# Optimization experiments

Measured on AMD Instinct MI355X. Metric: run time of the kernel, lower is better.

The kernel has to match this reference:

```python
import jax, jax.numpy as jnp
import numpy as np

HEAD_DIM = 512 // (8 * 2)  # in_dim // (num_heads * 2) = 32
SQRT2 = np.sqrt(2.0).astype(np.float32)


def dwt1d_haar(x):
    # Haar DWT along last dim: L=(even+odd)/sqrt2, H=(even-odd)/sqrt2
    xe, xo = x[..., 0::2], x[..., 1::2]
    return (xe + xo) / SQRT2, (xe - xo) / SQRT2


def idwt1d_haar(L, H):
    # Inverse: even=(L+H)/sqrt2, odd=(L-H)/sqrt2, interleaved
    even = (L + H) / SQRT2
    odd = (L - H) / SQRT2
    x = jnp.stack([even, odd], axis=-1)  # [..., D/2, 2]
    return x.reshape(*x.shape[:-2], -1)  # [..., D]


def setup_inputs() -> dict:
    key = jax.random.key(0)
    k1, k2, k3, k4 = jax.random.split(key, 4)
    B, S, D = 8, 2048, 512
    queries = jax.random.normal(k1, (B, S, D), dtype=jnp.float32)
    keys = jax.random.normal(k2, (B, S, D), dtype=jnp.float32)
    values = jax.random.normal(k3, (B, S, D), dtype=jnp.float32)
    W_o = jax.random.normal(k4, (D, D), dtype=jnp.float32) * (1.0 / np.sqrt(D))
    b_o = jnp.zeros((D,), dtype=jnp.float32)
    return {"queries": queries, "keys": keys, "values": values, "W_o": W_o, "b_o": b_o}


def reference(queries, keys, values, W_o, b_o):
    scale = 1.0 / jnp.sqrt(jnp.asarray(HEAD_DIM, dtype=queries.dtype))
    q_L, q_H = dwt1d_haar(queries)
    k_L, k_H = dwt1d_haar(keys)
    v_L, v_H = dwt1d_haar(values)
    # [B,S,S] score matrices for each wavelet branch
    attn_L = jax.nn.softmax(jnp.einsum("bqd,bkd->bqk", q_L, k_L) * scale, axis=-1)
    attn_H = jax.nn.softmax(jnp.einsum("bqd,bkd->bqk", q_H, k_H) * scale, axis=-1)
    L_out = jnp.einsum("bqk,bkd->bqd", attn_L, v_L)
    H_out = jnp.einsum("bqk,bkd->bqd", attn_H, v_H)
    output = idwt1d_haar(L_out, H_out)  # [B,S,D]
    return output @ W_o.T + b_o
```

## Files before the change

### kernel.cpp

```cpp
#include <hip/hip_runtime.h>

#define INV_SQRT2 0.70710678118654752f
#define QSCALE    0.17677669529663689f
#define LOG2E     1.44269504088896340f
#define SM_HALF   16.0f

typedef __attribute__((ext_vector_type(8))) short bf16x8;
typedef __attribute__((ext_vector_type(4))) float f32x4;
typedef __attribute__((ext_vector_type(16))) float f32x16;

__device__ __forceinline__ unsigned cvt_pk_bf16(float a, float b) {
  unsigned r;
  asm("v_cvt_pk_bf16_f32 %0, %1, %2" : "=v"(r) : "v"(a), "v"(b));
  return r;
}

__device__ __forceinline__ float exp2_raw(float x) {
  float r;
  asm("v_exp_f32 %0, %1" : "=v"(r) : "v"(x));
  return r;
}

__device__ __forceinline__ void async16(const short* g, short* l) {
  typedef __attribute__((address_space(3))) unsigned lds_u32;
  typedef const __attribute__((address_space(1))) unsigned glb_u32;
  __builtin_amdgcn_global_load_lds((glb_u32*)g, (lds_u32*)l, 16, 0, 0);
}

__launch_bounds__(256, 4)
__global__ void dwt_all(const float* __restrict__ q, const float* __restrict__ k,
                        const float* __restrict__ v, const float* __restrict__ W,
                        short* __restrict__ qs, short* __restrict__ ks,
                        short* __restrict__ vt, short* __restrict__ w2) {
  __shared__ float tL[32][65];
  __shared__ float tH[32][65];
  int bi = blockIdx.x;
  int t = threadIdx.x;
  if (bi < 2048) {
    int idx = bi * 256 + t;
    int j = idx & 31;
    int s = (idx >> 5) & 2047;
    int b = idx >> 16;
    const float4* qp = (const float4*)(q + ((size_t)(b * 2048 + s)) * 512 + j * 16);
    const float4* kp = (const float4*)(k + ((size_t)(b * 2048 + s)) * 512 + j * 16);
    float4 a0 = qp[0], a1 = qp[1], a2 = qp[2], a3 = qp[3];
    float4 c0 = kp[0], c1 = kp[1], c2 = kp[2], c3 = kp[3];
    union { bf16x8 v; unsigned u[4]; } qL, qH, kL, kH;
    const float cs = INV_SQRT2 * QSCALE * LOG2E;
    qL.u[0] = cvt_pk_bf16((a0.x + a0.y) * cs, (a0.z + a0.w) * cs);
    qL.u[1] = cvt_pk_bf16((a1.x + a1.y) * cs, (a1.z + a1.w) * cs);
    qL.u[2] = cvt_pk_bf16((a2.x + a2.y) * cs, (a2.z + a2.w) * cs);
    qL.u[3] = cvt_pk_bf16((a3.x + a3.y) * cs, (a3.z + a3.w) * cs);
    qH.u[0] = cvt_pk_bf16((a0.x - a0.y) * cs, (a0.z - a0.w) * cs);
    qH.u[1] = cvt_pk_bf16((a1.x - a1.y) * cs, (a1.z - a1.w) * cs);
    qH.u[2] = cvt_pk_bf16((a2.x - a2.y) * cs, (a2.z - a2.w) * cs);
    qH.u[3] = cvt_pk_bf16((a3.x - a3.y) * cs, (a3.z - a3.w) * cs);
    kL.u[0] = cvt_pk_bf16((c0.x + c0.y) * INV_SQRT2, (c0.z + c0.w) * INV_SQRT2);
    kL.u[1] = cvt_pk_bf16((c1.x + c1.y) * INV_SQRT2, (c1.z + c1.w) * INV_SQRT2);
    kL.u[2] = cvt_pk_bf16((c2.x + c2.y) * INV_SQRT2, (c2.z + c2.w) * INV_SQRT2);
    kL.u[3] = cvt_pk_bf16((c3.x + c3.y) * INV_SQRT2, (c3.z + c3.w) * INV_SQRT2);
    kH.u[0] = cvt_pk_bf16((c0.x - c0.y) * INV_SQRT2, (c0.z - c0.w) * INV_SQRT2);
    kH.u[1] = cvt_pk_bf16((c1.x - c1.y) * INV_SQRT2, (c1.z - c1.w) * INV_SQRT2);
    kH.u[2] = cvt_pk_bf16((c2.x - c2.y) * INV_SQRT2, (c2.z - c2.w) * INV_SQRT2);
    kH.u[3] = cvt_pk_bf16((c3.x - c3.y) * INV_SQRT2, (c3.z - c3.w) * INV_SQRT2);
    size_t oL = ((size_t)(b * 2) * 2048 + s) * 256 + j * 8;
    size_t oH = oL + (size_t)2048 * 256;
    *(bf16x8*)(qs + oL) = qL.v;  *(bf16x8*)(qs + oH) = qH.v;
    *(bf16x8*)(ks + oL) = kL.v;  *(bf16x8*)(ks + oH) = kH.v;
  } else if (bi < 4096) {
    int bi2 = bi - 2048;
    int it = bi2 & 3, st = (bi2 >> 2) & 63, b = bi2 >> 8;
#pragma unroll
    for (int rep = 0; rep < 4; rep++) {
      int unit = rep * 256 + t;
      int r = unit >> 5, cp = (unit & 31) * 2;
      float4 vv = *(const float4*)(v + ((size_t)(b * 2048 + st * 32 + r)) * 512 + it * 128 + cp * 2);
      tL[r][cp]     = (vv.x + vv.y) * INV_SQRT2;
      tL[r][cp + 1] = (vv.z + vv.w) * INV_SQRT2;
      tH[r][cp]     = (vv.x - vv.y) * INV_SQRT2;
      tH[r][cp + 1] = (vv.z - vv.w) * INV_SQRT2;
    }
    __syncthreads();
    {
      int i = t >> 2, cc = t & 3;
      union { bf16x8 v; unsigned u[4]; } pL, pH;
#pragma unroll
      for (int p = 0; p < 4; p++) {
        pL.u[p] = cvt_pk_bf16(tL[cc * 8 + p * 2][i], tL[cc * 8 + p * 2 + 1][i]);
        pH.u[p] = cvt_pk_bf16(tH[cc * 8 + p * 2][i], tH[cc * 8 + p * 2 + 1][i]);
      }
      size_t o = ((size_t)(b * 2) * 256 + it * 64 + i) * 2048 + st * 32 + cc * 8;
      *(bf16x8*)(vt + o) = pL.v;
      *(bf16x8*)(vt + o + (size_t)256 * 2048) = pH.v;
    }
  } else {
    int idx = (bi - 4096) * 256 + t;
    int j = idx >> 6, i4 = (idx & 63) * 4;
    const float4* src = (const float4*)(W + (size_t)j * 512 + 2 * i4);
    float4 f0 = src[0], f1 = src[1];
    uint2 dl, dh;
    dl.x = cvt_pk_bf16((f0.x + f0.y) * INV_SQRT2, (f0.z + f0.w) * INV_SQRT2);
    dl.y = cvt_pk_bf16((f1.x + f1.y) * INV_SQRT2, (f1.z + f1.w) * INV_SQRT2);
    dh.x = cvt_pk_bf16((f0.x - f0.y) * INV_SQRT2, (f0.z - f0.w) * INV_SQRT2);
    dh.y = cvt_pk_bf16((f1.x - f1.y) * INV_SQRT2, (f1.z - f1.w) * INV_SQRT2);
    *(uint2*)(w2 + (size_t)j * 512 + i4) = dl;
    *(uint2*)(w2 + (size_t)j * 512 + 256 + i4) = dh;
  }
}

__launch_bounds__(256, 2)
__global__ void flash_attn(const short* __restrict__ qs, const short* __restrict__ ks,
                           const short* __restrict__ vt, short* __restrict__ os) {
  __shared__ short lds[36864];
  short* klds = lds;
  short* vlds = lds + 16384;
  short* plds = lds + 32768;

  int tid = threadIdx.x;
  int w = tid >> 6, L = tid & 63;
  int lq = L & 31, hi = L >> 5;
  int qt = w & 1, ct = w >> 1;
  int bb = blockIdx.x, qb = blockIdx.y;

  bf16x8 qf[16];
  const short* qptr = qs + (((size_t)bb * 2048) + qb * 64 + qt * 32 + lq) * 256 + hi * 8;
#pragma unroll
  for (int ksI = 0; ksI < 16; ksI++)
    qf[ksI] = *(const bf16x8*)(qptr + ksI * 16);

  f32x16 oacc[4];
#pragma unroll
  for (int mt = 0; mt < 4; mt++)
#pragma unroll
    for (int i = 0; i < 16; i++) oacc[mt][i] = 0.f;
  float l_i = 0.f;

  const short* kbase = ks + ((size_t)bb * 2048) * 256;
  const short* vbase = vt + ((size_t)bb * 256) * 2048;

  int krow = ct * 32 + lq, ksw = krow & 7;
  int qrow = qt * 32 + lq, qsw = qrow & 7;
  int sw8 = lq & 7;

  const short* kaddr[16];
#pragma unroll
  for (int i = 0; i < 16; i++)
    kaddr[i] = klds + krow * 256 + (((i << 1) | hi) ^ ksw) * 8;
  short* pwr[4];
#pragma unroll
  for (int g = 0; g < 4; g++)
    pwr[g] = plds + qrow * 64 + ((4 * ct + g) ^ qsw) * 8 + hi * 4;
  const short* prdA[4];
  const short* prdB[4];
#pragma unroll
  for (int i = 0; i < 4; i++) {
    int ch = (((i << 1) | hi) ^ sw8) * 8;
    prdA[i] = plds + lq * 64 + ch;
    prdB[i] = plds + (32 + lq) * 64 + ch;
  }
  int vch[4];
#pragma unroll
  for (int i = 0; i < 4; i++)
    vch[i] = (((i << 1) | hi) ^ sw8) * 8;
  const short* vrowp[2];
#pragma unroll
  for (int dt = 0; dt < 2; dt++)
    vrowp[dt] = vlds + (w * 64 + dt * 32 + lq) * 64;

  const short* kp[8];
  const short* vp[8];
#pragma unroll
  for (int rep = 0; rep < 8; rep++) {
    int o = w * 8 + rep;
    int r = 2 * o + (L >> 5);
    int c = (L & 31) ^ (r & 7);
    kp[rep] = kbase + r * 256 + c * 8;
    int n = 8 * o + (L >> 3);
    int cv = (L & 7) ^ (n & 7);
    vp[rep] = vbase + n * 2048 + cv * 8;
  }

#pragma unroll
  for (int rep = 0; rep < 8; rep++) {
    async16(kp[rep], klds + (w * 8 + rep) * 512);
    kp[rep] += 16384;
  }
  __syncthreads();

  for (int kt = 0; kt < 32; kt++) {
#pragma unroll
    for (int rep = 0; rep < 8; rep++) {
      async16(vp[rep], vlds + (w * 8 + rep) * 512);
      vp[rep] += 64;
    }

    f32x16 s0, s1;
#pragma unroll
    for (int i = 0; i < 16; i++) { s0[i] = -SM_HALF; s1[i] = -SM_HALF; }
    __builtin_amdgcn_s_setprio(1);
#pragma unroll
    for (int ksI = 0; ksI < 16; ksI += 2) {
      bf16x8 kb0 = *(const bf16x8*)kaddr[ksI];
      bf16x8 kb1 = *(const bf16x8*)kaddr[ksI + 1];
      s0 = __builtin_amdgcn_mfma_f32_32x32x16_bf16(kb0, qf[ksI], s0, 0, 0, 0);
      s1 = __builtin_amdgcn_mfma_f32_32x32x16_bf16(kb1, qf[ksI + 1], s1, 0, 0, 0);
    }
    __builtin_amdgcn_s_setprio(0);

    float rs = 0.f;
#pragma unroll
    for (int g = 0; g < 4; g++) {
      float p0 = exp2_raw(s0[4 * g]     + s1[4 * g]);
      float p1 = exp2_raw(s0[4 * g + 1] + s1[4 * g + 1]);
      float p2 = exp2_raw(s0[4 * g + 2] + s1[4 * g + 2]);
      float p3 = exp2_raw(s0[4 * g + 3] + s1[4 * g + 3]);
      rs += (p0 + p1) + (p2 + p3);
      uint2 d; d.x = cvt_pk_bf16(p0, p1); d.y = cvt_pk_bf16(p2, p3);
      *(uint2*)pwr[g] = d;
    }
    l_i += rs;
    __syncthreads();

    if (kt < 31) {
#pragma unroll
      for (int rep = 0; rep < 8; rep++) {
        async16(kp[rep], klds + (w * 8 + rep) * 512);
        kp[rep] += 16384;
      }
    }

    bf16x8 pa[4], pb[4];
#pragma unroll
    for (int i = 0; i < 4; i++) {
      pa[i] = *(const bf16x8*)prdA[i];
      pb[i] = *(const bf16x8*)prdB[i];
    }
    __builtin_amdgcn_s_setprio(1);
#pragma unroll
    for (int dt = 0; dt < 2; dt++) {
#pragma unroll
      for (int i = 0; i < 4; i++) {
        bf16x8 vb = *(const bf16x8*)(vrowp[dt] + vch[i]);
        oacc[dt * 2]     = __builtin_amdgcn_mfma_f32_32x32x16_bf16(vb, pa[i], oacc[dt * 2], 0, 0, 0);
        oacc[dt * 2 + 1] = __builtin_amdgcn_mfma_f32_32x32x16_bf16(vb, pb[i], oacc[dt * 2 + 1], 0, 0, 0);
      }
    }
    __builtin_amdgcn_s_setprio(0);
    __syncthreads();
  }

  float lt = l_i + __shfl_xor(l_i, 32, 64);
  float* lbuf = (float*)plds;
  if (hi == 0) lbuf[(ct * 2 + qt) * 32 + lq] = lt;
  __syncthreads();
  float inv0 = 1.f / (lbuf[lq] + lbuf[64 + lq]);
  float inv1 = 1.f / (lbuf[32 + lq] + lbuf[96 + lq]);

#pragma unroll
  for (int ot = 0; ot < 4; ot++) {
    int qt2 = ot & 1, dt = ot >> 1;
    float inv = qt2 ? inv1 : inv0;
    int qg = qt2 * 32 + lq;
#pragma unroll
    for (int g = 0; g < 4; g++) {
      uint2 d;
      d.x = cvt_pk_bf16(oacc[ot][4 * g] * inv, oacc[ot][4 * g + 1] * inv);
      d.y = cvt_pk_bf16(oacc[ot][4 * g + 2] * inv, oacc[ot][4 * g + 3] * inv);
      *(uint2*)(lds + qg * 264 + w * 64 + dt * 32 + 8 * g + 4 * hi) = d;
    }
  }
  __syncthreads();
  short* obase = os + (((size_t)bb * 2048) + qb * 64) * 256;
#pragma unroll
  for (int rep = 0; rep < 8; rep++) {
    int cid = rep * 256 + tid;
    int row = cid >> 5, c = cid & 31;
    *(bf16x8*)(obase + row * 256 + c * 8) = *(const bf16x8*)(lds + row * 264 + c * 8);
  }
}

__launch_bounds__(256, 2)
__global__ void out_gemm(const short* __restrict__ os, const short* __restrict__ w2,
                         const float* __restrict__ bo, float* __restrict__ out) {
  __shared__ short alds[2][8192];
  __shared__ short blds[2][8192];
  int tid = threadIdx.x;
  int w = tid >> 6, L = tid & 63, lo = L & 15, hi = L >> 4;
  int wr = w >> 1, wc = w & 1;
  int br = blockIdx.x, bc = blockIdx.y;

  int rrow[4], rchk[4];
#pragma unroll
  for (int rep = 0; rep < 4; rep++) {
    int o = w * 4 + rep;
    int r = o * 8 + (L >> 3);
    rrow[rep] = r;
    rchk[rep] = ((L & 7) ^ (r & 7)) * 8;
  }
  int b = br >> 4;
  int s0 = (br & 15) * 128;
  const short* abase = os + ((size_t)(b * 2) * 2048 + s0) * 256;
  const short* bbase = w2 + (size_t)(bc * 128) * 512;

  f32x4 acc[4][4];
#pragma unroll
  for (int mt = 0; mt < 4; mt++)
#pragma unroll
    for (int nt = 0; nt < 4; nt++)
      acc[mt][nt] = (f32x4){0.f, 0.f, 0.f, 0.f};

  int fch[2];
#pragma unroll
  for (int kc = 0; kc < 2; kc++)
    fch[kc] = ((kc * 4 + hi) ^ (lo & 7)) * 8;

#pragma unroll
  for (int rep = 0; rep < 4; rep++) {
    async16(abase + rrow[rep] * 256 + rchk[rep], &alds[0][(w * 4 + rep) * 512] + L * 8);
    async16(bbase + rrow[rep] * 512 + rchk[rep], &blds[0][(w * 4 + rep) * 512] + L * 8);
  }
  __syncthreads();

  int p = 0;
  for (int kt = 0; kt < 8; kt++) {
    if (kt < 7) {
      int k1 = kt + 1;
      int half = k1 >> 2, i0 = (k1 & 3) * 64;
      const short* ab = abase + (size_t)half * 2048 * 256 + i0;
#pragma unroll
      for (int rep = 0; rep < 4; rep++) {
        async16(ab + rrow[rep] * 256 + rchk[rep], &alds[p ^ 1][(w * 4 + rep) * 512] + L * 8);
        async16(bbase + rrow[rep] * 512 + k1 * 64 + rchk[rep], &blds[p ^ 1][(w * 4 + rep) * 512] + L * 8);
      }
    }
    bf16x8 af[4], bfr[4];
#pragma unroll
    for (int kc = 0; kc < 2; kc++) {
#pragma unroll
      for (int mt = 0; mt < 4; mt++)
        af[mt] = *(const bf16x8*)(&alds[p][(wr * 64 + mt * 16 + lo) * 64 + fch[kc]]);
#pragma unroll
      for (int nt = 0; nt < 4; nt++)
        bfr[nt] = *(const bf16x8*)(&blds[p][(wc * 64 + nt * 16 + lo) * 64 + fch[kc]]);
#pragma unroll
      for (int mt = 0; mt < 4; mt++)
#pragma unroll
        for (int nt = 0; nt < 4; nt++)
          acc[mt][nt] = __builtin_amdgcn_mfma_f32_16x16x32_bf16(af[mt], bfr[nt], acc[mt][nt], 0, 0, 0);
    }
    __syncthreads();
    p ^= 1;
  }

#pragma unroll
  for (int nt = 0; nt < 4; nt++) {
    int cc = bc * 128 + wc * 64 + nt * 16 + lo;
    float bias = bo[cc];
#pragma unroll
    for (int mt = 0; mt < 4; mt++) {
      int rrbase = br * 128 + wr * 64 + mt * 16 + hi * 4;
#pragma unroll
      for (int r = 0; r < 4; r++)
        out[(size_t)(rrbase + r) * 512 + cc] = acc[mt][nt][r] + bias;
    }
  }
}

extern "C" void kernel_launch(void* const* d_in, const int* in_sizes, int n_in,
                              void* d_out, int out_size, void* d_ws, size_t ws_size,
                              hipStream_t stream) {
  const float* q  = (const float*)d_in[0];
  const float* k  = (const float*)d_in[1];
  const float* v  = (const float*)d_in[2];
  const float* W  = (const float*)d_in[3];
  const float* bo = (const float*)d_in[4];
  short* ws  = (short*)d_ws;
  short* qs  = ws;
  short* ksb = ws + (size_t)8  * 1024 * 1024;
  short* vtp = ws + (size_t)16 * 1024 * 1024;
  short* osb = ws + (size_t)24 * 1024 * 1024;
  short* w2  = ws + (size_t)32 * 1024 * 1024;

  dwt_all<<<4224, 256, 0, stream>>>(q, k, v, W, qs, ksb, vtp, w2);
  flash_attn<<<dim3(16, 32), 256, 0, stream>>>(qs, ksb, vtp, osb);
  out_gemm<<<dim3(128, 4), 256, 0, stream>>>(osb, w2, bo, (float*)d_out);
}
```

Measured before the change: 245.3 us.

## Load V fragments directly from global into registers, dropping the V LDS stage

The V tile is no longer staged through shared memory with async copies. Each wave now reads its own V fragments straight from global memory into registers, issued before the barrier, and feeds them to the PV MFMAs. This shrinks the LDS footprint and removes LDS write and read traffic for V. In exchange it adds global-load latency to the inner loop with no double buffering, and the barrier now waits only on LDS counters, so the V loads may stall the MFMAs.

```diff
diff --git a/kernel.cpp b/kernel.cpp
--- a/kernel.cpp
+++ b/kernel.cpp
@@ -111,10 +111,9 @@
 __launch_bounds__(256, 2)
 __global__ void flash_attn(const short* __restrict__ qs, const short* __restrict__ ks,
                            const short* __restrict__ vt, short* __restrict__ os) {
-  __shared__ short lds[36864];
+  __shared__ short lds[20480];
   short* klds = lds;
-  short* vlds = lds + 16384;
-  short* plds = lds + 32768;
+  short* plds = lds + 16384;
 
   int tid = threadIdx.x;
   int w = tid >> 6, L = tid & 63;
@@ -158,26 +157,17 @@
     prdA[i] = plds + lq * 64 + ch;
     prdB[i] = plds + (32 + lq) * 64 + ch;
   }
-  int vch[4];
-#pragma unroll
-  for (int i = 0; i < 4; i++)
-    vch[i] = (((i << 1) | hi) ^ sw8) * 8;
-  const short* vrowp[2];
-#pragma unroll
-  for (int dt = 0; dt < 2; dt++)
-    vrowp[dt] = vlds + (w * 64 + dt * 32 + lq) * 64;
+
+  const short* vga = vbase + (size_t)(w * 64 + lq) * 2048 + hi * 8;
+  const short* vgb = vga + (size_t)32 * 2048;
 
   const short* kp[8];
-  const short* vp[8];
 #pragma unroll
   for (int rep = 0; rep < 8; rep++) {
     int o = w * 8 + rep;
     int r = 2 * o + (L >> 5);
     int c = (L & 31) ^ (r & 7);
     kp[rep] = kbase + r * 256 + c * 8;
-    int n = 8 * o + (L >> 3);
-    int cv = (L & 7) ^ (n & 7);
-    vp[rep] = vbase + n * 2048 + cv * 8;
   }
 
 #pragma unroll
@@ -188,12 +178,6 @@
   __syncthreads();
 
   for (int kt = 0; kt < 32; kt++) {
-#pragma unroll
-    for (int rep = 0; rep < 8; rep++) {
-      async16(vp[rep], vlds + (w * 8 + rep) * 512);
-      vp[rep] += 64;
-    }
-
     f32x16 s0, s1;
 #pragma unroll
     for (int i = 0; i < 16; i++) { s0[i] = -SM_HALF; s1[i] = -SM_HALF; }
@@ -219,7 +203,19 @@
       *(uint2*)pwr[g] = d;
     }
     l_i += rs;
-    __syncthreads();
+
+    bf16x8 va0 = *(const bf16x8*)(vga + 0);
+    bf16x8 va1 = *(const bf16x8*)(vga + 16);
+    bf16x8 va2 = *(const bf16x8*)(vga + 32);
+    bf16x8 va3 = *(const bf16x8*)(vga + 48);
+    bf16x8 vB0 = *(const bf16x8*)(vgb + 0);
+    bf16x8 vB1 = *(const bf16x8*)(vgb + 16);
+    bf16x8 vB2 = *(const bf16x8*)(vgb + 32);
+    bf16x8 vB3 = *(const bf16x8*)(vgb + 48);
+    vga += 64; vgb += 64;
+
+    asm volatile("s_waitcnt lgkmcnt(0)" ::: "memory");
+    __builtin_amdgcn_s_barrier();
 
     if (kt < 31) {
 #pragma unroll
@@ -236,21 +232,28 @@
       pb[i] = *(const bf16x8*)prdB[i];
     }
     __builtin_amdgcn_s_setprio(1);
-#pragma unroll
-    for (int dt = 0; dt < 2; dt++) {
-#pragma unroll
-      for (int i = 0; i < 4; i++) {
-        bf16x8 vb = *(const bf16x8*)(vrowp[dt] + vch[i]);
-        oacc[dt * 2]     = __builtin_amdgcn_mfma_f32_32x32x16_bf16(vb, pa[i], oacc[dt * 2], 0, 0, 0);
-        oacc[dt * 2 + 1] = __builtin_amdgcn_mfma_f32_32x32x16_bf16(vb, pb[i], oacc[dt * 2 + 1], 0, 0, 0);
-      }
-    }
+    oacc[0] = __builtin_amdgcn_mfma_f32_32x32x16_bf16(va0, pa[0], oacc[0], 0, 0, 0);
+    oacc[1] = __builtin_amdgcn_mfma_f32_32x32x16_bf16(va0, pb[0], oacc[1], 0, 0, 0);
+    oacc[0] = __builtin_amdgcn_mfma_f32_32x32x16_bf16(va1, pa[1], oacc[0], 0, 0, 0);
+    oacc[1] = __builtin_amdgcn_mfma_f32_32x32x16_bf16(va1, pb[1], oacc[1], 0, 0, 0);
+    oacc[0] = __builtin_amdgcn_mfma_f32_32x32x16_bf16(va2, pa[2], oacc[0], 0, 0, 0);
+    oacc[1] = __builtin_amdgcn_mfma_f32_32x32x16_bf16(va2, pb[2], oacc[1], 0, 0, 0);
+    oacc[0] = __builtin_amdgcn_mfma_f32_32x32x16_bf16(va3, pa[3], oacc[0], 0, 0, 0);
+    oacc[1] = __builtin_amdgcn_mfma_f32_32x32x16_bf16(va3, pb[3], oacc[1], 0, 0, 0);
+    oacc[2] = __builtin_amdgcn_mfma_f32_32x32x16_bf16(vB0, pa[0], oacc[2], 0, 0, 0);
+    oacc[3] = __builtin_amdgcn_mfma_f32_32x32x16_bf16(vB0, pb[0], oacc[3], 0, 0, 0);
+    oacc[2] = __builtin_amdgcn_mfma_f32_32x32x16_bf16(vB1, pa[1], oacc[2], 0, 0, 0);
+    oacc[3] = __builtin_amdgcn_mfma_f32_32x32x16_bf16(vB1, pb[1], oacc[3], 0, 0, 0);
+    oacc[2] = __builtin_amdgcn_mfma_f32_32x32x16_bf16(vB2, pa[2], oacc[2], 0, 0, 0);
+    oacc[3] = __builtin_amdgcn_mfma_f32_32x32x16_bf16(vB2, pb[2], oacc[3], 0, 0, 0);
+    oacc[2] = __builtin_amdgcn_mfma_f32_32x32x16_bf16(vB3, pa[3], oacc[2], 0, 0, 0);
+    oacc[3] = __builtin_amdgcn_mfma_f32_32x32x16_bf16(vB3, pb[3], oacc[3], 0, 0, 0);
     __builtin_amdgcn_s_setprio(0);
     __syncthreads();
   }
 
   float lt = l_i + __shfl_xor(l_i, 32, 64);
-  float* lbuf = (float*)plds;
+  float* lbuf = (float*)(lds + 20224);
   if (hi == 0) lbuf[(ct * 2 + qt) * 32 + lq] = lt;
   __syncthreads();
   float inv0 = 1.f / (lbuf[lq] + lbuf[64 + lq]);
```

Result: slower. 266.3 us (+8.5%).
